# Performance work log

Hardware: AMD Instinct MI355X
Metric: run time of the kernel (lower is better)

The kernel has to match this reference:

```python
import jax, jax.numpy as jnp
import numpy as np

# cfg constants (ProposalLayerSoft.__init__)
GRID_SIZE = jnp.array([8000.0, 8000.0, 2000.0], dtype=jnp.float32)   # MULTI_PERSON.SPACE_SIZE (mm)
CUBE_SIZE = jnp.array([128.0, 128.0, 64.0], dtype=jnp.float32)       # MULTI_PERSON.INITIAL_CUBE_SIZE
GRID_CENTER = jnp.array([0.0, 0.0, 300.0], dtype=jnp.float32)        # MULTI_PERSON.SPACE_CENTER
NUM_CAND = 10                                                         # MULTI_PERSON.MAX_PEOPLE_NUM
THRESHOLD = 0.3                                                       # MULTI_PERSON.THRESHOLD


def setup_inputs() -> dict:
    key = jax.random.key(0)
    # root heatmap cube in [0,1): [B, X, Y, Z]
    root_cubes = jax.random.uniform(key, (32, 128, 128, 64), dtype=jnp.float32)
    return {"root_cubes": root_cubes}


def _nms_topk(x):
    """3x3x3 max-pool peak suppression + top-k (repo's nms()).
    x: [B, X, Y, Z] -> (values [B,K], unravel_index [B,K,3] float)."""
    B, X, Y, Z = x.shape
    pooled = jax.lax.reduce_window(
        x, -jnp.inf, jax.lax.max,
        window_dimensions=(1, 3, 3, 3),
        window_strides=(1, 1, 1, 1),
        padding=[(0, 0), (1, 1), (1, 1), (1, 1)],
    )
    peaks = jnp.where(x == pooled, x, 0.0)           # keep only local maxima
    flat = peaks.reshape(B, X * Y * Z)
    topk_values, topk_index = jax.lax.top_k(flat, NUM_CAND)
    # C-order unravel (matches repo's get_index)
    ix = topk_index // (Y * Z)
    iy = (topk_index % (Y * Z)) // Z
    iz = topk_index % Z
    idx = jnp.stack([ix, iy, iz], axis=-1).astype(jnp.float32)  # [B, K, 3]
    return topk_values, idx


def reference(root_cubes):
    x = jax.lax.stop_gradient(root_cubes)  # original calls .detach()
    topk_values, topk_index = _nms_topk(x)
    # get_real_loc: voxel index -> world coords (mm)
    loc = topk_index / (CUBE_SIZE - 1.0) * GRID_SIZE + GRID_CENTER - GRID_SIZE / 2.0
    conf = (topk_values > THRESHOLD).astype(jnp.float32) - 1.0  # col 3
    grid_centers = jnp.concatenate(
        [loc, conf[..., None], topk_values[..., None]], axis=-1
    )  # [B, K, 5]: (x, y, z, valid_flag, score)
    return grid_centers
```

## Files before the change

### kernel.cpp

```cpp
#include <hip/hip_runtime.h>
#include <stdint.h>


#define TPB 256
#define IT 14
#define TILES 10
#define NK 10
#define WCAP 256
typedef unsigned long long u64;

__device__ __forceinline__ u64 bfly_max_u64(u64 v) {
#pragma unroll
  for (int off = 1; off < 64; off <<= 1) {
    u64 o = __shfl_xor(v, off, 64);
    v = (o > v) ? o : v;
  }
  return v;
}

__global__ __launch_bounds__(TPB, 5) void peaks_topk(
    const float* __restrict__ in, u64* __restrict__ part) {
  __shared__ __align__(16) float4 ymb[2][2][TPB];
  __shared__ u64 cand[4][WCAP];
  __shared__ int cnt[4];
  __shared__ u64 wtop[4 * NK];

  const int tid = threadIdx.x;
  const int x = tid >> 4, y = tid & 15;
  const int w = tid >> 6, lane = tid & 63;
  const int bx = blockIdx.x, by = blockIdx.y, b = blockIdx.z;

  if (lane == 0) cnt[w] = 0;
#pragma unroll
  for (int i = 0; i < WCAP / 64; ++i) cand[w][lane + 64 * i] = 0;

  const int gx = bx * IT + x - 1;
  const int gy = by * IT + y - 1;
  const int cx = min(127, max(0, gx));
  const int cy = min(127, max(0, gy));
  const float* __restrict__ col =
      in + ((size_t)b << 20) + (size_t)(((cx << 7) | cy) << 6);
  const bool interior =
      (x >= 1) && (x <= IT) && (y >= 1) && (y <= IT) && (gx <= 127) && (gy <= 127);

  float4 cur0 = *(const float4*)(col);
  float4 cur1 = *(const float4*)(col + 4);
  float prev_last = -1e30f;

#pragma unroll 1
  for (int q = 0; q < 8; ++q) {
    float4 nxt0, nxt1;
    if (q < 7) {
      nxt0 = *(const float4*)(col + (q + 1) * 8);
      nxt1 = *(const float4*)(col + (q + 1) * 8 + 4);
    } else {
      nxt0 = make_float4(-1e30f, -1e30f, -1e30f, -1e30f);
      nxt1 = nxt0;
    }
    float v[8] = {cur0.x, cur0.y, cur0.z, cur0.w,
                  cur1.x, cur1.y, cur1.z, cur1.w};
    float zm[8];
    zm[0] = fmaxf(prev_last, fmaxf(v[0], v[1]));
#pragma unroll
    for (int j = 1; j < 7; ++j) zm[j] = fmaxf(v[j - 1], fmaxf(v[j], v[j + 1]));
    zm[7] = fmaxf(v[6], fmaxf(v[7], nxt0.x));
    float ym[8];
#pragma unroll
    for (int j = 0; j < 8; ++j) {
      float a = __shfl_up(zm[j], 1, 64);
      float c = __shfl_down(zm[j], 1, 64);
      ym[j] = fmaxf(zm[j], fmaxf(a, c));
    }
    const int buf = q & 1;
    ymb[buf][0][tid] = make_float4(ym[0], ym[1], ym[2], ym[3]);
    ymb[buf][1][tid] = make_float4(ym[4], ym[5], ym[6], ym[7]);
    __syncthreads();
    if (interior) {
      float4 a0 = ymb[buf][0][tid - 16];
      float4 b0 = ymb[buf][0][tid + 16];
      float4 a1 = ymb[buf][1][tid - 16];
      float4 b1 = ymb[buf][1][tid + 16];
      float am[8] = {a0.x, a0.y, a0.z, a0.w, a1.x, a1.y, a1.z, a1.w};
      float bm[8] = {b0.x, b0.y, b0.z, b0.w, b1.x, b1.y, b1.z, b1.w};
#pragma unroll
      for (int j = 0; j < 8; ++j) {
        float m27 = fmaxf(ym[j], fmaxf(am[j], bm[j]));
        if (v[j] >= m27) {
          unsigned g = ((unsigned)gx << 13) | ((unsigned)gy << 6) |
                       (unsigned)(q * 8 + j);
          u64 key = ((u64)__float_as_uint(v[j]) << 32) | (u64)(unsigned)(~g);
          int s = atomicAdd(&cnt[w], 1);
          if (s < WCAP) cand[w][s] = key;
        }
      }
    }
    prev_last = v[7];
    cur0 = nxt0;
    cur1 = nxt1;
  }

  {
    __builtin_amdgcn_s_waitcnt(0);
    u64 c0 = cand[w][lane];
    u64 c1 = cand[w][lane + 64];
    u64 c2 = cand[w][lane + 128];
    u64 c3 = cand[w][lane + 192];
    u64 mine = 0;
#pragma unroll 1
    for (int r = 0; r < NK; ++r) {
      u64 b01 = (c0 > c1) ? c0 : c1;
      u64 b23 = (c2 > c3) ? c2 : c3;
      u64 best = (b01 > b23) ? b01 : b23;
      u64 m = bfly_max_u64(best);
      if (m != 0 && best == m) {
        if (c0 == m) c0 = 0;
        else if (c1 == m) c1 = 0;
        else if (c2 == m) c2 = 0;
        else c3 = 0;
      }
      if (lane == r) mine = m;
    }
    if (lane < NK) wtop[w * NK + lane] = mine;
  }
  __syncthreads();

  if (w == 0) {
    u64 c0 = (lane < 4 * NK) ? wtop[lane] : 0;
    u64 mine = 0;
#pragma unroll 1
    for (int r = 0; r < NK; ++r) {
      u64 m = bfly_max_u64(c0);
      if (m != 0 && c0 == m) c0 = 0;
      if (lane == r) mine = m;
    }
    if (lane < NK)
      part[((size_t)b * (TILES * TILES) + (size_t)(by * TILES + bx)) * NK +
           lane] = mine;
  }
}

__global__ __launch_bounds__(TPB) void final_select(
    const u64* __restrict__ part, float* __restrict__ out) {
  __shared__ u64 cand[1024];
  __shared__ u64 red4[4];
  const int tid = threadIdx.x;
  const int b = blockIdx.x;
  const int w = tid >> 6, lane = tid & 63;
  const int NKEY = TILES * TILES * NK;

  const u64* __restrict__ src = part + (size_t)b * NKEY;
  for (int i = tid; i < 1024; i += TPB) cand[i] = (i < NKEY) ? src[i] : 0;
  __syncthreads();

  for (int r = 0; r < NK; ++r) {
    u64 best = 0;
    int slot = -1;
#pragma unroll
    for (int k = 0; k < 4; ++k) {
      int i = tid + k * TPB;
      if (cand[i] > best) { best = cand[i]; slot = i; }
    }
    u64 wm = bfly_max_u64(best);
    if (lane == 0) red4[w] = wm;
    __syncthreads();
    u64 win = red4[0];
#pragma unroll
    for (int k = 1; k < 4; ++k) win = (red4[k] > win) ? red4[k] : win;
    if (win != 0 && best == win && slot >= 0) cand[slot] = 0;
    if (tid == 0) {
      float val = 0.0f;
      unsigned g = 0u;
      if (win != 0) {
        val = __uint_as_float((unsigned)(win >> 32));
        g = ~((unsigned)win);
      }
      float fx = (float)(g >> 13) * (8000.0f / 127.0f) - 4000.0f;
      float fy = (float)((g >> 6) & 127u) * (8000.0f / 127.0f) - 4000.0f;
      float fz = (float)(g & 63u) * (2000.0f / 63.0f) - 700.0f;
      float conf = (val > 0.3f) ? 0.0f : -1.0f;
      float* o = out + ((size_t)b * NK + r) * 5;
      o[0] = fx; o[1] = fy; o[2] = fz; o[3] = conf; o[4] = val;
    }
    __syncthreads();
  }
}

extern "C" void kernel_launch(void* const* d_in, const int* in_sizes, int n_in,
                              void* d_out, int out_size, void* d_ws, size_t ws_size,
                              hipStream_t stream) {
  const float* in = (const float*)d_in[0];
  float* out = (float*)d_out;
  u64* part = (u64*)d_ws;

  const int B = in_sizes[0] >> 20;
  dim3 gridA(TILES, TILES, (unsigned)B);
  peaks_topk<<<gridA, dim3(TPB), 0, stream>>>(in, part);
  final_select<<<dim3((unsigned)B), dim3(TPB), 0, stream>>>(part, out);
}
```

Baseline: 241.5 us.

## Restructure peak search into per-wave register sliding window with per-lane top-k

Each wave now owns a 16x8 column tile with lanes mapped to z. It slides along x, keeping three y-max planes in registers, and does the z-neighbour max with lane shuffles. This removes the shared-memory exchange, the per-step __syncthreads and the atomic candidate buffer. Each lane keeps a sorted top-10 in registers, merged across the wave by butterfly reductions. The trade-off is more halo reloads in y (10 loads for 8 rows), fewer and larger blocks, and higher register pressure.

```diff
diff --git a/kernel.cpp b/kernel.cpp
--- a/kernel.cpp
+++ b/kernel.cpp
@@ -3,10 +3,12 @@
 
 
 #define TPB 256
-#define IT 14
-#define TILES 10
 #define NK 10
-#define WCAP 256
+#define WX 16
+#define WY 8
+#define GX 8
+#define GY 4
+#define WAVES_PER_B (GX * GY * 4)
 typedef unsigned long long u64;
 
 __device__ __forceinline__ u64 bfly_max_u64(u64 v) {
@@ -18,145 +20,110 @@
   return v;
 }
 
-__global__ __launch_bounds__(TPB, 5) void peaks_topk(
+__global__ __launch_bounds__(TPB, 4) void peaks_topk(
     const float* __restrict__ in, u64* __restrict__ part) {
-  __shared__ __align__(16) float4 ymb[2][2][TPB];
-  __shared__ u64 cand[4][WCAP];
-  __shared__ int cnt[4];
-  __shared__ u64 wtop[4 * NK];
-
   const int tid = threadIdx.x;
-  const int x = tid >> 4, y = tid & 15;
   const int w = tid >> 6, lane = tid & 63;
   const int bx = blockIdx.x, by = blockIdx.y, b = blockIdx.z;
+  const int x0 = bx * WX;
+  const int y0 = (by * 4 + w) * WY;
+  const float* __restrict__ src = in + ((size_t)b << 20) + lane;
 
-  if (lane == 0) cnt[w] = 0;
+  u64 top[NK];
 #pragma unroll
-  for (int i = 0; i < WCAP / 64; ++i) cand[w][lane + 64 * i] = 0;
+  for (int i = 0; i < NK; ++i) top[i] = 0;
 
-  const int gx = bx * IT + x - 1;
-  const int gy = by * IT + y - 1;
-  const int cx = min(127, max(0, gx));
-  const int cy = min(127, max(0, gy));
-  const float* __restrict__ col =
-      in + ((size_t)b << 20) + (size_t)(((cx << 7) | cy) << 6);
-  const bool interior =
-      (x >= 1) && (x <= IT) && (y >= 1) && (y <= IT) && (gx <= 127) && (gy <= 127);
+  float ymP[WY], ymC[WY], ymN[WY], vC[WY], vN[WY];
 
-  float4 cur0 = *(const float4*)(col);
-  float4 cur1 = *(const float4*)(col + 4);
-  float prev_last = -1e30f;
+  auto colpass = [&](int x, float* ym, float* vrow) {
+    float v[WY + 2], zm[WY + 2];
+    const int cx = min(127, max(0, x));
+#pragma unroll
+    for (int j = 0; j < WY + 2; ++j) {
+      const int cy = min(127, max(0, y0 - 1 + j));
+      v[j] = src[(size_t)(((cx << 7) | cy) << 6)];
+    }
+#pragma unroll
+    for (int j = 0; j < WY + 2; ++j) {
+      float a = __shfl_up(v[j], 1, 64);
+      float c = __shfl_down(v[j], 1, 64);
+      zm[j] = fmaxf(v[j], fmaxf(a, c));
+    }
+#pragma unroll
+    for (int j = 0; j < WY; ++j) {
+      ym[j] = fmaxf(zm[j], fmaxf(zm[j + 1], zm[j + 2]));
+      vrow[j] = v[j + 1];
+    }
+  };
 
-#pragma unroll 1
-  for (int q = 0; q < 8; ++q) {
-    float4 nxt0, nxt1;
-    if (q < 7) {
-      nxt0 = *(const float4*)(col + (q + 1) * 8);
-      nxt1 = *(const float4*)(col + (q + 1) * 8 + 4);
-    } else {
-      nxt0 = make_float4(-1e30f, -1e30f, -1e30f, -1e30f);
-      nxt1 = nxt0;
-    }
-    float v[8] = {cur0.x, cur0.y, cur0.z, cur0.w,
-                  cur1.x, cur1.y, cur1.z, cur1.w};
-    float zm[8];
-    zm[0] = fmaxf(prev_last, fmaxf(v[0], v[1]));
+  colpass(x0 - 1, ymP, vN);
+  colpass(x0, ymC, vC);
+
+#pragma unroll 2
+  for (int xi = 0; xi < WX; ++xi) {
+    colpass(x0 + xi + 1, ymN, vN);
 #pragma unroll
-    for (int j = 1; j < 7; ++j) zm[j] = fmaxf(v[j - 1], fmaxf(v[j], v[j + 1]));
-    zm[7] = fmaxf(v[6], fmaxf(v[7], nxt0.x));
-    float ym[8];
+    for (int j = 0; j < WY; ++j) {
+      float m27 = fmaxf(ymP[j], fmaxf(ymC[j], ymN[j]));
+      if (vC[j] >= m27) {
+        unsigned g = ((unsigned)(x0 + xi) << 13) | ((unsigned)(y0 + j) << 6) |
+                     (unsigned)lane;
+        u64 key = ((u64)__float_as_uint(vC[j]) << 32) | (u64)(unsigned)(~g);
+        if (key > top[NK - 1]) {
+          top[NK - 1] = key;
 #pragma unroll
-    for (int j = 0; j < 8; ++j) {
-      float a = __shfl_up(zm[j], 1, 64);
-      float c = __shfl_down(zm[j], 1, 64);
-      ym[j] = fmaxf(zm[j], fmaxf(a, c));
-    }
-    const int buf = q & 1;
-    ymb[buf][0][tid] = make_float4(ym[0], ym[1], ym[2], ym[3]);
-    ymb[buf][1][tid] = make_float4(ym[4], ym[5], ym[6], ym[7]);
-    __syncthreads();
-    if (interior) {
-      float4 a0 = ymb[buf][0][tid - 16];
-      float4 b0 = ymb[buf][0][tid + 16];
-      float4 a1 = ymb[buf][1][tid - 16];
-      float4 b1 = ymb[buf][1][tid + 16];
-      float am[8] = {a0.x, a0.y, a0.z, a0.w, a1.x, a1.y, a1.z, a1.w};
-      float bm[8] = {b0.x, b0.y, b0.z, b0.w, b1.x, b1.y, b1.z, b1.w};
-#pragma unroll
-      for (int j = 0; j < 8; ++j) {
-        float m27 = fmaxf(ym[j], fmaxf(am[j], bm[j]));
-        if (v[j] >= m27) {
-          unsigned g = ((unsigned)gx << 13) | ((unsigned)gy << 6) |
-                       (unsigned)(q * 8 + j);
-          u64 key = ((u64)__float_as_uint(v[j]) << 32) | (u64)(unsigned)(~g);
-          int s = atomicAdd(&cnt[w], 1);
-          if (s < WCAP) cand[w][s] = key;
+          for (int i = NK - 1; i > 0; --i) {
+            u64 a = top[i - 1], c = top[i];
+            bool sw = c > a;
+            top[i - 1] = sw ? c : a;
+            top[i] = sw ? a : c;
+          }
         }
       }
     }
-    prev_last = v[7];
-    cur0 = nxt0;
-    cur1 = nxt1;
+#pragma unroll
+    for (int j = 0; j < WY; ++j) {
+      ymP[j] = ymC[j];
+      ymC[j] = ymN[j];
+      vC[j] = vN[j];
+    }
   }
 
-  {
-    __builtin_amdgcn_s_waitcnt(0);
-    u64 c0 = cand[w][lane];
-    u64 c1 = cand[w][lane + 64];
-    u64 c2 = cand[w][lane + 128];
-    u64 c3 = cand[w][lane + 192];
-    u64 mine = 0;
+  u64 mine = 0;
 #pragma unroll 1
-    for (int r = 0; r < NK; ++r) {
-      u64 b01 = (c0 > c1) ? c0 : c1;
-      u64 b23 = (c2 > c3) ? c2 : c3;
-      u64 best = (b01 > b23) ? b01 : b23;
-      u64 m = bfly_max_u64(best);
-      if (m != 0 && best == m) {
-        if (c0 == m) c0 = 0;
-        else if (c1 == m) c1 = 0;
-        else if (c2 == m) c2 = 0;
-        else c3 = 0;
-      }
-      if (lane == r) mine = m;
+  for (int r = 0; r < NK; ++r) {
+    u64 m = bfly_max_u64(top[0]);
+    if (m != 0 && top[0] == m) {
+#pragma unroll
+      for (int i = 0; i < NK - 1; ++i) top[i] = top[i + 1];
+      top[NK - 1] = 0;
     }
-    if (lane < NK) wtop[w * NK + lane] = mine;
+    if (lane == r) mine = m;
   }
-  __syncthreads();
-
-  if (w == 0) {
-    u64 c0 = (lane < 4 * NK) ? wtop[lane] : 0;
-    u64 mine = 0;
-#pragma unroll 1
-    for (int r = 0; r < NK; ++r) {
-      u64 m = bfly_max_u64(c0);
-      if (m != 0 && c0 == m) c0 = 0;
-      if (lane == r) mine = m;
-    }
-    if (lane < NK)
-      part[((size_t)b * (TILES * TILES) + (size_t)(by * TILES + bx)) * NK +
-           lane] = mine;
+  if (lane < NK) {
+    const int widx = (by * 4 + w) * GX + bx;
+    part[((size_t)b * WAVES_PER_B + (size_t)widx) * NK + lane] = mine;
   }
 }
 
 __global__ __launch_bounds__(TPB) void final_select(
     const u64* __restrict__ part, float* __restrict__ out) {
-  __shared__ u64 cand[1024];
+  __shared__ u64 cand[WAVES_PER_B * NK];
   __shared__ u64 red4[4];
   const int tid = threadIdx.x;
   const int b = blockIdx.x;
   const int w = tid >> 6, lane = tid & 63;
-  const int NKEY = TILES * TILES * NK;
+  const int NKEY = WAVES_PER_B * NK;
 
   const u64* __restrict__ src = part + (size_t)b * NKEY;
-  for (int i = tid; i < 1024; i += TPB) cand[i] = (i < NKEY) ? src[i] : 0;
+  for (int i = tid; i < NKEY; i += TPB) cand[i] = src[i];
   __syncthreads();
 
   for (int r = 0; r < NK; ++r) {
     u64 best = 0;
     int slot = -1;
 #pragma unroll
-    for (int k = 0; k < 4; ++k) {
+    for (int k = 0; k < NKEY / TPB; ++k) {
       int i = tid + k * TPB;
       if (cand[i] > best) { best = cand[i]; slot = i; }
     }
@@ -193,7 +160,7 @@
   u64* part = (u64*)d_ws;
 
   const int B = in_sizes[0] >> 20;
-  dim3 gridA(TILES, TILES, (unsigned)B);
+  dim3 gridA(GX, GY, (unsigned)B);
   peaks_topk<<<gridA, dim3(TPB), 0, stream>>>(in, part);
   final_select<<<dim3((unsigned)B), dim3(TPB), 0, stream>>>(part, out);
 }
```

Measured after the change: 271.5 us. 12.5% more time.
